# Optimization experiments

Measured on AMD Instinct MI355X. Metric: run time of the kernel, lower is better.

Reference implementation:

```python
import jax, jax.numpy as jnp
import numpy as np

H = 256       # hiddenDim
E = 300       # embDim
VOCAB = 50000
S = 1024      # number of sentences in document
L = 64        # words per sentence (chain-tree depth)
TOPIC = 100
TARGET = 5


def setup_inputs() -> dict:
    key = jax.random.key(0)
    ks = jax.random.split(key, 21)
    f32 = jnp.float32
    return {
        'sentenceInIndex': jax.random.randint(ks[0], (S, L), 0, VOCAB),
        'depTypes': jax.random.randint(ks[1], (S, L - 1), 0, 9),
        'D_T_distr': jax.random.uniform(ks[2], (TOPIC,), dtype=f32),
        'h0': jax.random.normal(ks[3], (H,), dtype=f32),
        'idx2vec': jax.random.normal(ks[4], (VOCAB, E), dtype=f32) * 0.1,
        'q': jax.random.normal(ks[5], (10, H), dtype=f32) * 0.1,
        'W': jax.random.normal(ks[6], (3 * H, E), dtype=f32) * 0.05,
        'U': jax.random.normal(ks[7], (3 * H, H), dtype=f32) * 0.05,
        'D': jax.random.normal(ks[8], (3 * H, H), dtype=f32) * 0.05,
        'b': jax.random.normal(ks[9], (3 * H,), dtype=f32) * 0.05,
        'gru_wih': jax.random.normal(ks[10], (3 * H, H), dtype=f32) * 0.05,
        'gru_whh': jax.random.normal(ks[11], (3 * H, H), dtype=f32) * 0.05,
        'gru_bih': jax.random.normal(ks[12], (3 * H,), dtype=f32) * 0.05,
        'gru_bhh': jax.random.normal(ks[13], (3 * H,), dtype=f32) * 0.05,
        'gate_W': jax.random.normal(ks[14], (2 * H, H), dtype=f32) * 0.05,
        'gate_U': jax.random.normal(ks[15], (2 * H, H), dtype=f32) * 0.05,
        'gate_b': jax.random.normal(ks[16], (2 * H,), dtype=f32) * 0.05,
        'mlp_W': jax.random.normal(ks[17], (H, TOPIC), dtype=f32) * 0.05,
        'mlp_b': jax.random.normal(ks[18], (H,), dtype=f32) * 0.05,
        'out_W': jax.random.normal(ks[19], (TARGET, H), dtype=f32) * 0.05,
        'out_b': jax.random.normal(ks[20], (TARGET,), dtype=f32) * 0.05,
    }


def reference(sentenceInIndex, depTypes, D_T_distr, h0, idx2vec, q, W, U, D, b,
              gru_wih, gru_whh, gru_bih, gru_bhh,
              gate_W, gate_U, gate_b, mlp_W, mlp_b, out_W, out_b):
    # ---- DERNN over chain-canonicalized dependency trees (vectorized over S sentences) ----
    x = idx2vec[sentenceInIndex]                        # [S, L, E] gather
    Wx = jnp.einsum('sle,ke->slk', x, W)                # [S, L, 3H]
    qe = q[depTypes]                                    # [S, L-1, H] dep-type embeddings for edges k->k+1
    Dq = jnp.einsum('slh,kh->slk', qe, D)               # [S, L-1, 3H]

    # leaf node (position L-1): q_sum = q[-1] ('leafNotion'); no child h term
    dq_leaf = D @ q[-1]                                 # [3H]
    iu_leaf = Wx[:, -1, H:] + dq_leaf[H:] + b[H:]       # [S, 2H]
    h = jnp.tanh(jax.nn.sigmoid(iu_leaf[:, :H]) * jnp.tanh(iu_leaf[:, H:]))  # [S, H]

    # internal nodes k = L-2 .. 0, single child k+1 (edge k)
    pre = Wx[:, :L - 1] + Dq + b                        # [S, L-1, 3H]
    pre_rev = jnp.swapaxes(pre[:, ::-1], 0, 1)          # [L-1, S, 3H] bottom-up order

    def tree_step(h_c, pre_k):
        tot = pre_k + h_c @ U.T                         # [S, 3H]
        f = jax.nn.sigmoid(tot[:, :H]) * h_c            # child forget gate * child h (single child => sum)
        i = jax.nn.sigmoid(tot[:, H:2 * H])
        u = jnp.tanh(tot[:, 2 * H:])
        h_n = jnp.tanh(i * u + f)
        return h_n, None

    sentenceVector, _ = jax.lax.scan(tree_step, h, pre_rev)  # [S, H] root hidden per sentence

    # ---- GRU over sentence sequence (batch 1), torch nn.GRU math ----
    def gru_step(hh, xt):
        gi = gru_wih @ xt + gru_bih                     # [3H]
        gh = gru_whh @ hh + gru_bhh
        r = jax.nn.sigmoid(gi[:H] + gh[:H])
        z = jax.nn.sigmoid(gi[H:2 * H] + gh[H:2 * H])
        n = jnp.tanh(gi[2 * H:] + r * gh[2 * H:])
        return (1.0 - z) * n + z * hh, None

    hT, _ = jax.lax.scan(gru_step, h0, sentenceVector)  # [H] final hidden state

    # ---- topic vector, GATE fusion, classifier ----
    t = jnp.tanh(mlp_W @ D_T_distr + mlp_b)             # [H]
    g = gate_W @ hT + gate_U @ t + gate_b               # [2H]
    v = jnp.tanh(jax.nn.sigmoid(g[:H]) * hT + jax.nn.sigmoid(g[H:]) * t)
    return jax.nn.softmax(out_W @ v + out_b)            # [TARGET]
```

## Files before the change

kernel.cpp:

```cpp
#include <hip/hip_runtime.h>

typedef short short8 __attribute__((ext_vector_type(8)));
typedef float f4 __attribute__((ext_vector_type(4)));
typedef int i4 __attribute__((ext_vector_type(4)));
typedef _Float16 half8 __attribute__((ext_vector_type(8)));
typedef _Float16 h2 __attribute__((ext_vector_type(2)));

#define HD 256
#define ED 300
#define EP 320
#define TH 768
#define NS 1024
#define LW 64
#define SH 4.5f

__device__ __forceinline__ unsigned short f2bf(float f) {
    unsigned int u = __float_as_uint(f);
    u = (u + 0x7FFFu + ((u >> 16) & 1u)) >> 16;
    return (unsigned short)u;
}
__device__ __forceinline__ float bf2f(unsigned short s) {
    return __uint_as_float(((unsigned int)s) << 16);
}
__device__ __forceinline__ float sigm(float x) {
    return __builtin_amdgcn_rcpf(1.f + __expf(-x));
}
__device__ __forceinline__ float tanh_(float x) {
    x = fminf(fmaxf(x, -15.f), 15.f);
    return 1.f - 2.f * __builtin_amdgcn_rcpf(1.f + __expf(2.f * x));
}
__device__ __forceinline__ unsigned int pack_h2(float a, float b) {
    h2 p; p.x = (_Float16)a; p.y = (_Float16)b;
    return __builtin_bit_cast(unsigned int, p);
}

__device__ __forceinline__ void load8bf(const unsigned short* p, float* o) {
    uint4 a = *(const uint4*)p;
    o[0] = bf2f((unsigned short)(a.x & 0xffff)); o[1] = bf2f((unsigned short)(a.x >> 16));
    o[2] = bf2f((unsigned short)(a.y & 0xffff)); o[3] = bf2f((unsigned short)(a.y >> 16));
    o[4] = bf2f((unsigned short)(a.z & 0xffff)); o[5] = bf2f((unsigned short)(a.z >> 16));
    o[6] = bf2f((unsigned short)(a.w & 0xffff)); o[7] = bf2f((unsigned short)(a.w >> 16));
}
__device__ __forceinline__ void ubf4(uint2 a, float* o) {
    o[0] = bf2f((unsigned short)(a.x & 0xffff)); o[1] = bf2f((unsigned short)(a.x >> 16));
    o[2] = bf2f((unsigned short)(a.y & 0xffff)); o[3] = bf2f((unsigned short)(a.y >> 16));
}

__device__ __forceinline__ int dot4(int a, int b, int c) {
#if __has_builtin(__builtin_amdgcn_sdot4)
    return __builtin_amdgcn_sdot4(a, b, c, false);
#else
    int s = c;
    s += (int)(signed char)(a & 0xff)        * (int)(signed char)(b & 0xff);
    s += (int)(signed char)((a >> 8) & 0xff) * (int)(signed char)((b >> 8) & 0xff);
    s += (int)(signed char)((a >> 16) & 0xff)* (int)(signed char)((b >> 16) & 0xff);
    s += (int)(signed char)((a >> 24) & 0xff)* (int)(signed char)((b >> 24) & 0xff);
    return s;
#endif
}

__device__ __forceinline__ i4 gload16(const signed char* p) {
    i4 r;
    asm volatile("global_load_dwordx4 %0, %1, off\n\ts_waitcnt vmcnt(0)"
                 : "=v"(r) : "v"(p));
    return r;
}

__global__ void k_prep(const float* __restrict__ W, const float* __restrict__ U,
                       const float* __restrict__ Wih, const float* __restrict__ Whh,
                       const float* __restrict__ q, const float* __restrict__ Dm,
                       const float* __restrict__ DT, const float* __restrict__ mlpW,
                       const float* __restrict__ mlpb,
                       const float* __restrict__ bih, const float* __restrict__ bhh,
                       unsigned short* __restrict__ Wb, _Float16* __restrict__ Uh,
                       _Float16* __restrict__ Wihh,
                       signed char* __restrict__ Wq, float* __restrict__ rowscale,
                       float* __restrict__ bias2,
                       float* __restrict__ Dq, float* __restrict__ tv) {
    __shared__ float smax[4];
    int bid = blockIdx.x, tid = threadIdx.x;
    if (bid < 768) {
        int r = bid;
        for (int j = tid; j < EP; j += 256)
            Wb[r * EP + j] = (j < ED) ? f2bf(W[r * ED + j]) : (unsigned short)0;
        float whv = Whh[r * HD + tid];
        for (int j = tid; j < HD; j += 256) {
            Uh[r * HD + j] = (_Float16)U[r * HD + j];
            Wihh[r * HD + j] = (_Float16)Wih[r * HD + j];
        }
        float v = fabsf(whv);
        for (int o = 32; o; o >>= 1) v = fmaxf(v, __shfl_xor(v, o));
        if ((tid & 63) == 0) smax[tid >> 6] = v;
        __syncthreads();
        float am = fmaxf(fmaxf(smax[0], smax[1]), fmaxf(smax[2], smax[3]));
        float inv = (am > 0.f) ? 127.f / am : 0.f;
        int qi = (int)rintf(whv * inv);
        qi = max(-127, min(127, qi));
        Wq[r * HD + tid] = (signed char)qi;
        if (tid == 0) rowscale[r] = (am / 127.f) * (SH / 127.f);
    } else if (bid < 798) {
        int idx = bid - 768;
        int d = idx / 3, part = idx - d * 3;
        int n = part * 256 + tid;
        float s = 0.f;
        for (int h = 0; h < HD; ++h) s += Dm[n * HD + h] * q[d * HD + h];
        Dq[d * TH + n] = s;
    } else {
        if (tid < HD) {
            float s = 0.f;
            for (int k = 0; k < 100; ++k) s += mlpW[tid * 100 + k] * DT[k];
            tv[tid] = tanh_(s + mlpb[tid]);
        }
        for (int r = tid; r < TH; r += 256)
            bias2[r] = bih[r] + ((r < 512) ? bhh[r] : 0.f);
    }
}

#define XP 328
__launch_bounds__(256, 2)
__global__ void k_phaseB(const int* __restrict__ sIdx, const int* __restrict__ depT,
                         const float* __restrict__ emb, const unsigned short* __restrict__ Wb,
                         const float* __restrict__ Dq, const float* __restrict__ bias,
                         unsigned short* __restrict__ pre) {
    __shared__ float dq_s[10 * 772];
    __shared__ float b_s[TH];
    __shared__ int dep_s[32];
    __shared__ int idx_s[32];
    __shared__ __align__(16) unsigned short xbf[32 * XP];
    int tid = threadIdx.x;
    int c0 = blockIdx.x * 32;
    for (int i = tid; i < 10 * 768; i += 256) {
        int d = i / 768, n = i - d * 768;
        dq_s[d * 772 + n] = Dq[i];
    }
    for (int i = tid; i < TH; i += 256) b_s[i] = bias[i];
    if (tid < 32) {
        int m = c0 + tid;
        idx_s[tid] = sIdx[m];
        int l = m & 63, s = m >> 6;
        dep_s[tid] = (l == 63) ? 9 : depT[s * 63 + l];
    }
    __syncthreads();
    for (int i = tid; i < 32 * EP; i += 256) {
        int row = i / EP, col = i - row * EP;
        unsigned short v = 0;
        if (col < ED) v = f2bf(emb[(long)idx_s[row] * ED + col]);
        xbf[row * XP + col] = v;
    }
    __syncthreads();

    int lane = tid & 63;
    int w = tid >> 6;
    int quad = lane >> 4, l16 = lane & 15;

    f4 acc[2][12];
#pragma unroll
    for (int cs = 0; cs < 2; ++cs)
#pragma unroll
        for (int ms = 0; ms < 12; ++ms) acc[cs][ms] = (f4){0.f, 0.f, 0.f, 0.f};

    const unsigned short* wbase = Wb + (w * 192 + l16) * EP;

#pragma unroll
    for (int kt = 0; kt < 10; ++kt) {
        int k0 = kt * 32 + quad * 8;
        short8 bf0 = *(const short8*)&xbf[l16 * XP + k0];
        short8 bf1 = *(const short8*)&xbf[(16 + l16) * XP + k0];
#pragma unroll
        for (int ms = 0; ms < 12; ++ms) {
            short8 af = *(const short8*)(wbase + ms * 16 * EP + k0);
            acc[0][ms] = __builtin_amdgcn_mfma_f32_16x16x32_bf16(af, bf0, acc[0][ms], 0, 0, 0);
            acc[1][ms] = __builtin_amdgcn_mfma_f32_16x16x32_bf16(af, bf1, acc[1][ms], 0, 0, 0);
        }
    }

#pragma unroll
    for (int cs = 0; cs < 2; ++cs) {
        int xr = c0 + cs * 16 + l16;
        int dep = dep_s[cs * 16 + l16];
        unsigned short* prow = pre + (long)xr * TH;
#pragma unroll
        for (int ms = 0; ms < 12; ++ms) {
            int ncol = w * 192 + ms * 16 + quad * 4;
            f4 dq4 = *(const f4*)&dq_s[dep * 772 + ncol];
            f4 b4 = *(const f4*)&b_s[ncol];
            unsigned int lo = (unsigned int)f2bf(acc[cs][ms][0] + dq4[0] + b4[0]) |
                              ((unsigned int)f2bf(acc[cs][ms][1] + dq4[1] + b4[1]) << 16);
            unsigned int hi = (unsigned int)f2bf(acc[cs][ms][2] + dq4[2] + b4[2]) |
                              ((unsigned int)f2bf(acc[cs][ms][3] + dq4[3] + b4[3]) << 16);
            uint2 v; v.x = lo; v.y = hi;
            *(uint2*)(prow + ncol) = v;
        }
    }
}

__global__ void __launch_bounds__(768) k_phaseC(
                         const unsigned short* __restrict__ pre,
                         const _Float16* __restrict__ Uh,
                         const _Float16* __restrict__ Wihh,
                         const float* __restrict__ bias2,
                         float* __restrict__ gi) {
    __shared__ __align__(16) uint4 hfr[512];
    __shared__ __align__(16) float tot[16 * 772];
    int tid = threadIdx.x;
    int lane = tid & 63, w = tid >> 6, quad = lane >> 4, l16 = lane & 15;
    int s0 = blockIdx.x * 16;

    uint4 frag[32];
    {
        const _Float16* base = Uh + (w * 64 + l16) * HD;
#pragma unroll
        for (int t = 0; t < 4; ++t)
#pragma unroll
            for (int kt = 0; kt < 8; ++kt)
                frag[t * 8 + kt] = *(const uint4*)(base + t * 16 * HD + kt * 32 + quad * 8);
    }

    int us = tid >> 5;
    int jg = tid & 31;
    int j0 = jg * 8;
    int hcell = (j0 >> 5) * 64 + 16 * ((j0 >> 3) & 3) + us;
    uint4 hcp;

    if (tid < 512) {
        const unsigned short* prow = pre + ((long)(s0 + us) * LW + 63) * TH;
        float iv[8], uv[8], hcv[8];
        load8bf(prow + 256 + j0, iv);
        load8bf(prow + 512 + j0, uv);
#pragma unroll
        for (int r = 0; r < 8; ++r) hcv[r] = tanh_(sigm(iv[r]) * tanh_(uv[r]));
        hcp.x = pack_h2(hcv[0], hcv[1]); hcp.y = pack_h2(hcv[2], hcv[3]);
        hcp.z = pack_h2(hcv[4], hcv[5]); hcp.w = pack_h2(hcv[6], hcv[7]);
        hfr[hcell] = hcp;
    }
    __syncthreads();

    int mb = w * 64 + quad * 4;

    for (int step = 0; step < 63; ++step) {
        int l = 62 - step;
        uint2 praw[6];
        if (tid < 512) {
            const unsigned short* prow = pre + ((long)(s0 + us) * LW + l) * TH;
#pragma unroll
            for (int g = 0; g < 3; ++g) {
                praw[2 * g]     = *(const uint2*)(prow + g * 256 + j0);
                praw[2 * g + 1] = *(const uint2*)(prow + g * 256 + j0 + 4);
            }
        }
        f4 a0 = (f4){0,0,0,0}, a1 = (f4){0,0,0,0}, a2 = (f4){0,0,0,0}, a3 = (f4){0,0,0,0};
#pragma unroll
        for (int kt = 0; kt < 8; ++kt) {
            half8 b = __builtin_bit_cast(half8, hfr[kt * 64 + lane]);
            a0 = __builtin_amdgcn_mfma_f32_16x16x32_f16(__builtin_bit_cast(half8, frag[kt]), b, a0, 0, 0, 0);
            a1 = __builtin_amdgcn_mfma_f32_16x16x32_f16(__builtin_bit_cast(half8, frag[8 + kt]), b, a1, 0, 0, 0);
            a2 = __builtin_amdgcn_mfma_f32_16x16x32_f16(__builtin_bit_cast(half8, frag[16 + kt]), b, a2, 0, 0, 0);
            a3 = __builtin_amdgcn_mfma_f32_16x16x32_f16(__builtin_bit_cast(half8, frag[24 + kt]), b, a3, 0, 0, 0);
        }
        float* tr = tot + l16 * 772;
        *(f4*)&tr[mb] = a0;
        *(f4*)&tr[mb + 16] = a1;
        *(f4*)&tr[mb + 32] = a2;
        *(f4*)&tr[mb + 48] = a3;
        __syncthreads();
        if (tid < 512) {
            const float* ts = tot + us * 772;
            float hcv[8];
            h2 px = __builtin_bit_cast(h2, hcp.x); h2 py = __builtin_bit_cast(h2, hcp.y);
            h2 pz = __builtin_bit_cast(h2, hcp.z); h2 pw = __builtin_bit_cast(h2, hcp.w);
            hcv[0] = (float)px.x; hcv[1] = (float)px.y; hcv[2] = (float)py.x; hcv[3] = (float)py.y;
            hcv[4] = (float)pz.x; hcv[5] = (float)pz.y; hcv[6] = (float)pw.x; hcv[7] = (float)pw.y;
#pragma unroll
            for (int hf = 0; hf < 2; ++hf) {
                int jb = j0 + hf * 4;
                float pf[4], pi_[4], pu[4];
                ubf4(praw[hf], pf);
                ubf4(praw[2 + hf], pi_);
                ubf4(praw[4 + hf], pu);
                f4 tf = *(const f4*)&ts[jb];
                f4 ti = *(const f4*)&ts[256 + jb];
                f4 tu = *(const f4*)&ts[512 + jb];
#pragma unroll
                for (int r = 0; r < 4; ++r) {
                    float ff = tf[r] + pf[r];
                    float ii = ti[r] + pi_[r];
                    float uu = tu[r] + pu[r];
                    hcv[hf * 4 + r] = tanh_(sigm(ii) * tanh_(uu) + sigm(ff) * hcv[hf * 4 + r]);
                }
            }
            hcp.x = pack_h2(hcv[0], hcv[1]); hcp.y = pack_h2(hcv[2], hcv[3]);
            hcp.z = pack_h2(hcv[4], hcv[5]); hcp.w = pack_h2(hcv[6], hcv[7]);
            hfr[hcell] = hcp;
        }
        __syncthreads();
    }

    {
        const _Float16* base = Wihh + (w * 64 + l16) * HD;
#pragma unroll
        for (int t = 0; t < 4; ++t)
#pragma unroll
            for (int kt = 0; kt < 8; ++kt)
                frag[t * 8 + kt] = *(const uint4*)(base + t * 16 * HD + kt * 32 + quad * 8);
    }
    f4 a0 = (f4){0,0,0,0}, a1 = (f4){0,0,0,0}, a2 = (f4){0,0,0,0}, a3 = (f4){0,0,0,0};
#pragma unroll
    for (int kt = 0; kt < 8; ++kt) {
        half8 b = __builtin_bit_cast(half8, hfr[kt * 64 + lane]);
        a0 = __builtin_amdgcn_mfma_f32_16x16x32_f16(__builtin_bit_cast(half8, frag[kt]), b, a0, 0, 0, 0);
        a1 = __builtin_amdgcn_mfma_f32_16x16x32_f16(__builtin_bit_cast(half8, frag[8 + kt]), b, a1, 0, 0, 0);
        a2 = __builtin_amdgcn_mfma_f32_16x16x32_f16(__builtin_bit_cast(half8, frag[16 + kt]), b, a2, 0, 0, 0);
        a3 = __builtin_amdgcn_mfma_f32_16x16x32_f16(__builtin_bit_cast(half8, frag[24 + kt]), b, a3, 0, 0, 0);
    }
    float* go = gi + (long)(s0 + l16) * TH;
    f4 b0 = *(const f4*)(bias2 + mb);
    f4 b1 = *(const f4*)(bias2 + mb + 16);
    f4 b2 = *(const f4*)(bias2 + mb + 32);
    f4 b3 = *(const f4*)(bias2 + mb + 48);
    *(f4*)(go + mb) = a0 + b0;
    *(f4*)(go + mb + 16) = a1 + b1;
    *(f4*)(go + mb + 32) = a2 + b2;
    *(f4*)(go + mb + 48) = a3 + b3;
}

__global__ void __launch_bounds__(256, 1) k_gru(
                      const signed char* __restrict__ Wq, const float* __restrict__ rowscale,
                      const float* __restrict__ bhh,
                      const float* __restrict__ gi, const float* __restrict__ h0,
                      const float* __restrict__ tv,
                      const float* __restrict__ gateW, const float* __restrict__ gateU,
                      const float* __restrict__ gateb,
                      const float* __restrict__ outW, const float* __restrict__ outb,
                      float* __restrict__ out) {
    __shared__ __align__(16) int qd[2][64];
    __shared__ float hts[HD];
    __shared__ float sgs[512];
    __shared__ float vvs[HD];
    __shared__ float lg[8];

    int tid = threadIdx.x;
    int j = tid;

    i4 wr_[16], wz_[16], wn_[16];
    {
        const signed char* pr = Wq + (long)j * HD;
        const signed char* pz = Wq + (long)(256 + j) * HD;
        const signed char* pn = Wq + (long)(512 + j) * HD;
#pragma unroll
        for (int c = 0; c < 16; ++c) {
            wr_[c] = gload16(pr + c * 16);
            wz_[c] = gload16(pz + c * 16);
            wn_[c] = gload16(pn + c * 16);
        }
    }
    float rs_r = rowscale[j];
    float rs_z = rowscale[256 + j];
    float rs_n = rowscale[512 + j];
    float bn = bhh[512 + j];

    float hv = h0[j];
    {
        float hc = fminf(fmaxf(hv, -SH), SH);
        ((signed char*)qd[0])[j] = (signed char)(int)rintf(hc * (127.f / SH));
    }
    float pgr, pgz, pgn;
    {
        const float* g = gi + j;
        pgr = g[0]; pgz = g[256]; pgn = g[512];
    }
    asm volatile("s_waitcnt lgkmcnt(0)" ::: "memory");
    __builtin_amdgcn_s_barrier();

    for (int t = 0; t < NS; ++t) {
        int p = t & 1;
        float gr = pgr, gz = pgz, gn = pgn;
        {
            long tn = (t + 1 < NS) ? (long)(t + 1) : (long)(NS - 1);
            const float* g = gi + tn * TH + j;
            pgr = g[0]; pgz = g[256]; pgn = g[512];
        }
        int ar = 0, az = 0, an = 0;
#pragma unroll
        for (int c = 0; c < 16; ++c) {
            i4 hb = *(const i4*)&qd[p][c * 4];
            ar = dot4(hb[0], wr_[c][0], ar);
            ar = dot4(hb[1], wr_[c][1], ar);
            ar = dot4(hb[2], wr_[c][2], ar);
            ar = dot4(hb[3], wr_[c][3], ar);
            az = dot4(hb[0], wz_[c][0], az);
            az = dot4(hb[1], wz_[c][1], az);
            az = dot4(hb[2], wz_[c][2], az);
            az = dot4(hb[3], wz_[c][3], az);
            an = dot4(hb[0], wn_[c][0], an);
            an = dot4(hb[1], wn_[c][1], an);
            an = dot4(hb[2], wn_[c][2], an);
            an = dot4(hb[3], wn_[c][3], an);
        }
        float rv = sigm(gr + (float)ar * rs_r);
        float zv = sigm(gz + (float)az * rs_z);
        float nv = tanh_(gn + rv * ((float)an * rs_n + bn));
        hv = (1.f - zv) * nv + zv * hv;
        float hc = fminf(fmaxf(hv, -SH), SH);
        ((signed char*)qd[p ^ 1])[j] = (signed char)(int)rintf(hc * (127.f / SH));
        asm volatile("s_waitcnt lgkmcnt(0)" ::: "memory");
        __builtin_amdgcn_s_barrier();
    }

    hts[j] = hv;
    __syncthreads();
    for (int r = tid; r < 512; r += 256) {
        float s = gateb[r];
        for (int k = 0; k < HD; ++k)
            s += gateW[r * HD + k] * hts[k] + gateU[r * HD + k] * tv[k];
        sgs[r] = sigm(s);
    }
    __syncthreads();
    vvs[tid] = tanh_(sgs[tid] * hts[tid] + sgs[256 + tid] * tv[tid]);
    __syncthreads();
    if (tid < 5) {
        float s = outb[tid];
        for (int k = 0; k < HD; ++k) s += outW[tid * HD + k] * vvs[k];
        lg[tid] = s;
    }
    __syncthreads();
    if (tid == 0) {
        float m = lg[0];
        for (int i = 1; i < 5; ++i) m = fmaxf(m, lg[i]);
        float e[5], sum = 0.f;
        for (int i = 0; i < 5; ++i) { e[i] = __expf(lg[i] - m); sum += e[i]; }
        for (int i = 0; i < 5; ++i) out[i] = e[i] / sum;
    }
}

extern "C" void kernel_launch(void* const* d_in, const int* in_sizes, int n_in,
                              void* d_out, int out_size, void* d_ws, size_t ws_size,
                              hipStream_t stream) {
    (void)in_sizes; (void)n_in; (void)out_size; (void)ws_size;
    const int* sIdx = (const int*)d_in[0];
    const int* depT = (const int*)d_in[1];
    const float* DT = (const float*)d_in[2];
    const float* h0 = (const float*)d_in[3];
    const float* emb = (const float*)d_in[4];
    const float* q = (const float*)d_in[5];
    const float* W = (const float*)d_in[6];
    const float* U = (const float*)d_in[7];
    const float* Dm = (const float*)d_in[8];
    const float* b = (const float*)d_in[9];
    const float* Wih = (const float*)d_in[10];
    const float* Whh = (const float*)d_in[11];
    const float* bih = (const float*)d_in[12];
    const float* bhh = (const float*)d_in[13];
    const float* gateW = (const float*)d_in[14];
    const float* gateU = (const float*)d_in[15];
    const float* gateb = (const float*)d_in[16];
    const float* mlpW = (const float*)d_in[17];
    const float* mlpb = (const float*)d_in[18];
    const float* outW = (const float*)d_in[19];
    const float* outb = (const float*)d_in[20];

    char* ws = (char*)d_ws;
    unsigned short* Wb = (unsigned short*)ws;   ws += 768 * 320 * 2;
    _Float16* Uh = (_Float16*)ws;               ws += 768 * 256 * 2;
    _Float16* Wihh = (_Float16*)ws;             ws += 768 * 256 * 2;
    signed char* Wq = (signed char*)ws;         ws += 768 * 256;
    float* rowscale = (float*)ws;               ws += 768 * 4;
    float* bias2 = (float*)ws;                  ws += 768 * 4;
    float* Dq = (float*)ws;                     ws += 10 * 768 * 4;
    float* tv = (float*)ws;                     ws += 1024;
    ws = (char*)d_ws + ((((size_t)(ws - (char*)d_ws)) + 4095) & ~(size_t)4095);
    unsigned short* pre = (unsigned short*)ws;  ws += (size_t)65536 * 768 * 2;
    float* gi = (float*)ws;                     ws += (size_t)1024 * 768 * 4;

    k_prep<<<dim3(799), dim3(256), 0, stream>>>(W, U, Wih, Whh, q, Dm, DT, mlpW, mlpb,
                                                bih, bhh,
                                                Wb, Uh, Wihh, Wq, rowscale, bias2, Dq, tv);
    k_phaseB<<<dim3(2048), dim3(256), 0, stream>>>(sIdx, depT, emb, Wb, Dq, b, pre);
    k_phaseC<<<dim3(64), dim3(768), 0, stream>>>(pre, Uh, Wihh, bias2, gi);
    k_gru<<<dim3(1), dim3(256), 0, stream>>>(Wq, rowscale, bhh, gi, h0, tv,
                                             gateW, gateU, gateb, outW, outb, (float*)d_out);
}
```

Before: 1.296 ms.

## Split GRU recurrence K-dimension across two thread halves with readlane broadcast

The single-block GRU kernel now runs 512 threads. Each half holds half of the int8 weight rows and computes partial dot products over 128 of the hidden inputs. The hidden vector is broadcast through readlane instead of being read from LDS vectors, and the second half's partial sums are exchanged through shared memory. This halves the serial dot-product chain per step but adds a second barrier and an LDS reduction on every timestep.

```diff
diff --git a/kernel.cpp b/kernel.cpp
--- a/kernel.cpp
+++ b/kernel.cpp
@@ -323,7 +323,7 @@
     *(f4*)(go + mb + 48) = a3 + b3;
 }
 
-__global__ void __launch_bounds__(256, 1) k_gru(
+__global__ void __launch_bounds__(512, 1) k_gru(
                       const signed char* __restrict__ Wq, const float* __restrict__ rowscale,
                       const float* __restrict__ bhh,
                       const float* __restrict__ gi, const float* __restrict__ h0,
@@ -333,21 +333,26 @@
                       const float* __restrict__ outW, const float* __restrict__ outb,
                       float* __restrict__ out) {
     __shared__ __align__(16) int qd[2][64];
+    __shared__ int partB[3][256];
     __shared__ float hts[HD];
     __shared__ float sgs[512];
     __shared__ float vvs[HD];
     __shared__ float lg[8];
 
     int tid = threadIdx.x;
-    int j = tid;
-
-    i4 wr_[16], wz_[16], wn_[16];
+    int j = tid & 255;
+    int half = tid >> 8;
+    int lk = tid & 31;
+    bool owner = (half == 0);
+
+    i4 wr_[8], wz_[8], wn_[8];
     {
-        const signed char* pr = Wq + (long)j * HD;
-        const signed char* pz = Wq + (long)(256 + j) * HD;
-        const signed char* pn = Wq + (long)(512 + j) * HD;
-#pragma unroll
-        for (int c = 0; c < 16; ++c) {
+        const signed char* base = Wq + half * 128;
+        const signed char* pr = base + (long)j * HD;
+        const signed char* pz = base + (long)(256 + j) * HD;
+        const signed char* pn = base + (long)(512 + j) * HD;
+#pragma unroll
+        for (int c = 0; c < 8; ++c) {
             wr_[c] = gload16(pr + c * 16);
             wz_[c] = gload16(pz + c * 16);
             wn_[c] = gload16(pn + c * 16);
@@ -359,12 +364,10 @@
     float bn = bhh[512 + j];
 
     float hv = h0[j];
-    {
+    float pgr = 0.f, pgz = 0.f, pgn = 0.f;
+    if (owner) {
         float hc = fminf(fmaxf(hv, -SH), SH);
         ((signed char*)qd[0])[j] = (signed char)(int)rintf(hc * (127.f / SH));
-    }
-    float pgr, pgz, pgn;
-    {
         const float* g = gi + j;
         pgr = g[0]; pgz = g[256]; pgn = g[512];
     }
@@ -373,49 +376,54 @@
 
     for (int t = 0; t < NS; ++t) {
         int p = t & 1;
-        float gr = pgr, gz = pgz, gn = pgn;
-        {
+        int hvec = qd[p][half * 32 + lk];
+        int ar = 0, az = 0, an = 0;
+#pragma unroll
+        for (int c = 0; c < 8; ++c) {
+#pragma unroll
+            for (int q = 0; q < 4; ++q) {
+                int hs = __builtin_amdgcn_readlane(hvec, c * 4 + q);
+                ar = dot4(hs, wr_[c][q], ar);
+                az = dot4(hs, wz_[c][q], az);
+                an = dot4(hs, wn_[c][q], an);
+            }
+        }
+        float gr = 0.f, gz = 0.f, gn_ = 0.f;
+        if (!owner) {
+            partB[0][j] = ar; partB[1][j] = az; partB[2][j] = an;
+        } else {
+            gr = pgr; gz = pgz; gn_ = pgn;
             long tn = (t + 1 < NS) ? (long)(t + 1) : (long)(NS - 1);
             const float* g = gi + tn * TH + j;
             pgr = g[0]; pgz = g[256]; pgn = g[512];
         }
-        int ar = 0, az = 0, an = 0;
-#pragma unroll
-        for (int c = 0; c < 16; ++c) {
-            i4 hb = *(const i4*)&qd[p][c * 4];
-            ar = dot4(hb[0], wr_[c][0], ar);
-            ar = dot4(hb[1], wr_[c][1], ar);
-            ar = dot4(hb[2], wr_[c][2], ar);
-            ar = dot4(hb[3], wr_[c][3], ar);
-            az = dot4(hb[0], wz_[c][0], az);
-            az = dot4(hb[1], wz_[c][1], az);
-            az = dot4(hb[2], wz_[c][2], az);
-            az = dot4(hb[3], wz_[c][3], az);
-            an = dot4(hb[0], wn_[c][0], an);
-            an = dot4(hb[1], wn_[c][1], an);
-            an = dot4(hb[2], wn_[c][2], an);
-            an = dot4(hb[3], wn_[c][3], an);
-        }
-        float rv = sigm(gr + (float)ar * rs_r);
-        float zv = sigm(gz + (float)az * rs_z);
-        float nv = tanh_(gn + rv * ((float)an * rs_n + bn));
-        hv = (1.f - zv) * nv + zv * hv;
-        float hc = fminf(fmaxf(hv, -SH), SH);
-        ((signed char*)qd[p ^ 1])[j] = (signed char)(int)rintf(hc * (127.f / SH));
         asm volatile("s_waitcnt lgkmcnt(0)" ::: "memory");
         __builtin_amdgcn_s_barrier();
-    }
-
-    hts[j] = hv;
-    __syncthreads();
-    for (int r = tid; r < 512; r += 256) {
-        float s = gateb[r];
+        if (owner) {
+            int fr = ar + partB[0][j];
+            int fz = az + partB[1][j];
+            int fn = an + partB[2][j];
+            float rv = sigm(gr + (float)fr * rs_r);
+            float zv = sigm(gz + (float)fz * rs_z);
+            float nv = tanh_(gn_ + rv * ((float)fn * rs_n + bn));
+            hv = (1.f - zv) * nv + zv * hv;
+            float hc = fminf(fmaxf(hv, -SH), SH);
+            ((signed char*)qd[p ^ 1])[j] = (signed char)(int)rintf(hc * (127.f / SH));
+        }
+        asm volatile("s_waitcnt lgkmcnt(0)" ::: "memory");
+        __builtin_amdgcn_s_barrier();
+    }
+
+    if (owner) hts[j] = hv;
+    __syncthreads();
+    {
+        float s = gateb[tid];
         for (int k = 0; k < HD; ++k)
-            s += gateW[r * HD + k] * hts[k] + gateU[r * HD + k] * tv[k];
-        sgs[r] = sigm(s);
-    }
-    __syncthreads();
-    vvs[tid] = tanh_(sgs[tid] * hts[tid] + sgs[256 + tid] * tv[tid]);
+            s += gateW[tid * HD + k] * hts[k] + gateU[tid * HD + k] * tv[k];
+        sgs[tid] = sigm(s);
+    }
+    __syncthreads();
+    if (tid < HD) vvs[tid] = tanh_(sgs[tid] * hts[tid] + sgs[256 + tid] * tv[tid]);
     __syncthreads();
     if (tid < 5) {
         float s = outb[tid];
@@ -476,6 +484,6 @@
                                                 Wb, Uh, Wihh, Wq, rowscale, bias2, Dq, tv);
     k_phaseB<<<dim3(2048), dim3(256), 0, stream>>>(sIdx, depT, emb, Wb, Dq, b, pre);
     k_phaseC<<<dim3(64), dim3(768), 0, stream>>>(pre, Uh, Wihh, bias2, gi);
-    k_gru<<<dim3(1), dim3(256), 0, stream>>>(Wq, rowscale, bhh, gi, h0, tv,
+    k_gru<<<dim3(1), dim3(512), 0, stream>>>(Wq, rowscale, bhh, gi, h0, tv,
                                              gateW, gateU, gateb, outW, outb, (float*)d_out);
 }
```

Measured after the change: 1.517 ms. 1.17x slower.
